# Kernel optimization log

Measured on AMD Instinct MI355X. Metric: run time of the kernel, lower is better.

## Reference

```python
import jax, jax.numpy as jnp
import numpy as np

B, S, H, E = 2, 2048, 16, 64
INV_SCALE = 8.0  # sqrt(head_dim); forward divides scores by this


def setup_inputs() -> dict:
    key = jax.random.key(0)
    ks = jax.random.split(key, 10)
    return {
        "query": jax.random.normal(ks[0], (B, S, H, E), dtype=jnp.float32),
        "key": jax.random.normal(ks[1], (B, S, H, E), dtype=jnp.float32),
        "value": jax.random.normal(ks[2], (B, S, H, E), dtype=jnp.float32),
        "attn_mask": jax.random.randint(ks[3], (B, S), 0, 2, dtype=jnp.int32),
        "Wq": jax.random.normal(ks[4], (E, E), dtype=jnp.float32) / np.sqrt(E),
        "bq": jax.random.normal(ks[5], (E,), dtype=jnp.float32) * 0.02,
        "Wk": jax.random.normal(ks[6], (E, E), dtype=jnp.float32) / np.sqrt(E),
        "bk": jax.random.normal(ks[7], (E,), dtype=jnp.float32) * 0.02,
        "Wv": jax.random.normal(ks[8], (E, E), dtype=jnp.float32) / np.sqrt(E),
        "bv": jax.random.normal(ks[9], (E,), dtype=jnp.float32) * 0.02,
    }


def reference(query, key, value, attn_mask, Wq, bq, Wk, bk, Wv, bv):
    # Linear projections over the last (embed) dim; torch Linear: x @ W.T + b
    q = jnp.einsum('bshe,fe->bhsf', query, Wq) + bq  # [B,H,S,E] (permute 0,2,1,3 fused)
    k = jnp.einsum('bshe,fe->bhsf', key, Wk) + bk
    v = jnp.einsum('bshe,fe->bhsf', value, Wv) + bv
    scores = jnp.einsum('bhqe,bhke->bhqk', q, k) / INV_SCALE  # [B,H,S,S]
    # mask: positions where attn_mask == 0 get -inf, broadcast over (1,1,k_len)
    masked = attn_mask[:, None, None, :] == 0  # [B,1,1,S]
    scores = jnp.where(masked, -jnp.inf, scores)
    attn = jax.nn.softmax(scores, axis=-1)
    out = jnp.einsum('bhqk,bhke->bqhe', attn, v)  # permute back to [B,S,H,E]
    return out
```

## Files before the change

kernel.cpp:

```cpp
#include <hip/hip_runtime.h>


#define BATCH 2
#define SEQ   2048
#define NH    16
#define DE    64
#define LDP   72
#define LDOF  68
#define NKT   (SEQ / 64)
#define QT    256
#define LOG2E 1.44269504088896340736f

using bf16x8   = __attribute__((ext_vector_type(8))) __bf16;
using bf16x4   = __attribute__((ext_vector_type(4))) __bf16;
using floatx4  = __attribute__((ext_vector_type(4))) float;
using floatx16 = __attribute__((ext_vector_type(16))) float;
using ushortx4 = __attribute__((ext_vector_type(4))) unsigned short;
using ushortx8 = __attribute__((ext_vector_type(8))) unsigned short;

__device__ __forceinline__ ushortx4 cvt4(floatx4 f) {
    bf16x4 h = __builtin_convertvector(f, bf16x4);
    return __builtin_bit_cast(ushortx4, h);
}

__device__ __forceinline__ void glds16(const unsigned short* g, unsigned short* l) {
    __builtin_amdgcn_global_load_lds(
        (const __attribute__((address_space(1))) unsigned int*)g,
        (__attribute__((address_space(3))) unsigned int*)l, 16, 0, 0);
}

__global__ __launch_bounds__(256) void proj_kernel(
    const float* __restrict__ xq, const float* __restrict__ xk, const float* __restrict__ xv,
    const float* __restrict__ Wq, const float* __restrict__ bq,
    const float* __restrict__ Wk, const float* __restrict__ bk,
    const float* __restrict__ Wv, const float* __restrict__ bv,
    unsigned short* __restrict__ qb, unsigned short* __restrict__ kb,
    unsigned short* __restrict__ vtb)
{
    __shared__ __align__(16) unsigned short Xb[64 * LDP];
    __shared__ __align__(16) unsigned short Wb[64 * LDP];
    __shared__ __align__(16) unsigned short Ob[64 * LDP];
    __shared__ float blds[64];

    const int t  = threadIdx.x;
    const int p  = blockIdx.x >> 10;
    const int bh = (blockIdx.x >> 5) & 31;
    const int st = blockIdx.x & 31;
    const int s0 = st * 64;
    const int b  = bh >> 4, h = bh & 15;
    const int lane = t & 63, w = t >> 6, quad = lane >> 4, l16 = lane & 15;

    const float* x    = (p == 0) ? xq : (p == 1) ? xk : xv;
    const float* W    = (p == 0) ? Wq : (p == 1) ? Wk : Wv;
    const float* bias = (p == 0) ? bq : (p == 1) ? bk : bv;

    #pragma unroll
    for (int i = 0; i < 4; ++i) {
        int idx = i * 1024 + t * 4;
        int row = idx >> 6, col = idx & 63;
        floatx4 xv4 = *(const floatx4*)(x + (((size_t)(b * SEQ + s0 + row) * NH + h) * DE + col));
        *(ushortx4*)&Xb[row * LDP + col] = cvt4(xv4);
        floatx4 wv4 = *(const floatx4*)(W + row * 64 + col);
        *(ushortx4*)&Wb[row * LDP + col] = cvt4(wv4);
    }
    if (t < 64) blds[t] = bias[t];
    __syncthreads();

    if (p < 2) {
        bf16x8 a0 = *(const bf16x8*)&Wb[(w * 16 + l16) * LDP + quad * 8];
        bf16x8 a1 = *(const bf16x8*)&Wb[(w * 16 + l16) * LDP + 32 + quad * 8];
        floatx4 bf4 = *(const floatx4*)&blds[w * 16 + quad * 4];
        const float scale = (p == 0) ? 0.125f * LOG2E : 1.0f;
        #pragma unroll
        for (int nb = 0; nb < 4; ++nb) {
            bf16x8 b0 = *(const bf16x8*)&Xb[(nb * 16 + l16) * LDP + quad * 8];
            bf16x8 b1 = *(const bf16x8*)&Xb[(nb * 16 + l16) * LDP + 32 + quad * 8];
            floatx4 c = {0.f, 0.f, 0.f, 0.f};
            c = __builtin_amdgcn_mfma_f32_16x16x32_bf16(a0, b0, c, 0, 0, 0);
            c = __builtin_amdgcn_mfma_f32_16x16x32_bf16(a1, b1, c, 0, 0, 0);
            floatx4 v;
            v[0] = (c[0] + bf4[0]) * scale; v[1] = (c[1] + bf4[1]) * scale;
            v[2] = (c[2] + bf4[2]) * scale; v[3] = (c[3] + bf4[3]) * scale;
            *(ushortx4*)&Ob[(nb * 16 + l16) * LDP + w * 16 + quad * 4] = cvt4(v);
        }
    } else {
        bf16x8 a0 = *(const bf16x8*)&Xb[(w * 16 + l16) * LDP + quad * 8];
        bf16x8 a1 = *(const bf16x8*)&Xb[(w * 16 + l16) * LDP + 32 + quad * 8];
        #pragma unroll
        for (int nb = 0; nb < 4; ++nb) {
            bf16x8 b0 = *(const bf16x8*)&Wb[(nb * 16 + l16) * LDP + quad * 8];
            bf16x8 b1 = *(const bf16x8*)&Wb[(nb * 16 + l16) * LDP + 32 + quad * 8];
            floatx4 c = {0.f, 0.f, 0.f, 0.f};
            c = __builtin_amdgcn_mfma_f32_16x16x32_bf16(a0, b0, c, 0, 0, 0);
            c = __builtin_amdgcn_mfma_f32_16x16x32_bf16(a1, b1, c, 0, 0, 0);
            float bw = blds[nb * 16 + l16];
            floatx4 v;
            v[0] = c[0] + bw; v[1] = c[1] + bw; v[2] = c[2] + bw; v[3] = c[3] + bw;
            *(ushortx4*)&Ob[(nb * 16 + l16) * LDP + w * 16 + quad * 4] = cvt4(v);
        }
    }
    __syncthreads();

    #pragma unroll
    for (int j = 0; j < 2; ++j) {
        int idx = j * 256 + t;
        int row = idx >> 3, c = idx & 7;
        int cp  = (c ^ (row & 7)) * 8;
        ushortx8 v = *(const ushortx8*)&Ob[row * LDP + c * 8];
        if (p < 2) {
            unsigned short* dst = (p == 0) ? qb : kb;
            *(ushortx8*)(dst + ((size_t)bh * SEQ + s0 + row) * DE + cp) = v;
        } else {
            *(ushortx8*)(vtb + ((size_t)bh * DE + row) * SEQ + s0 + cp) = v;
        }
    }
}

__global__ __launch_bounds__(512) void attn_kernel(
    const unsigned short* __restrict__ qb, const unsigned short* __restrict__ kb,
    const unsigned short* __restrict__ vtb, const int* __restrict__ mask,
    float* __restrict__ out)
{
    __shared__ __align__(16) char smem[16384 + 16384 + 36864 + 512];
    unsigned short* Kl = (unsigned short*)smem;
    unsigned short* Vl = (unsigned short*)(smem + 16384);
    unsigned short* Pq = (unsigned short*)(smem + 32768);
    float*          Ml = (float*)(smem + 32768 + 36864);
    float*          Ol = (float*)smem;

    const int t  = threadIdx.x;
    const int qt = blockIdx.x, bh = blockIdx.y;
    const int b  = bh >> 4, h = bh & 15;
    const int q0 = qt * QT;
    const int lane = t & 63, w = t >> 6;
    const int l31 = lane & 31, hl = lane >> 5;
    const int sw  = l31 & 7;
    const int qrow = w * 32 + l31;

    const unsigned short* kbase = kb + (size_t)bh * SEQ * DE;
    const unsigned short* vbase = vtb + (size_t)bh * DE * SEQ;
    const unsigned short* qsrc  = qb + ((size_t)bh * SEQ + q0) * DE;
    const int* mrow = mask + b * SEQ;

    #pragma unroll
    for (int u = 0; u < 4; ++u)
        glds16(qsrc + (u * 8 + w) * 512 + lane * 8, Pq + (u * 8 + w) * 512);
    glds16(kbase + (size_t)(w * 8 + (lane >> 3)) * DE + (lane & 7) * 8,  Kl + w * 512);
    glds16(vbase + (size_t)(w * 8 + (lane >> 3)) * SEQ + (lane & 7) * 8, Vl + w * 512);
    if (t < 64) Ml[t] = mrow[t] ? -16.0f : -1e30f;
    int mreg = (t < 64) ? mrow[64 + t] : 0;
    __syncthreads();

    bf16x8 qf[4];
    #pragma unroll
    for (int estep = 0; estep < 4; ++estep)
        qf[estep] = *(const bf16x8*)&Pq[qrow * 64 + (((2 * estep + hl) ^ sw) * 8)];

    float l_i = 0.f;
    floatx16 oacc[2];
    #pragma unroll
    for (int eh = 0; eh < 2; ++eh)
        #pragma unroll
        for (int r = 0; r < 16; ++r) oacc[eh][r] = 0.f;
    __syncthreads();

    for (int kt = 0; kt < NKT; ++kt) {
        const int cur = kt & 1, nxt = cur ^ 1;
        const unsigned short* Kc = Kl + cur * 4096;
        const unsigned short* Vc = Vl + cur * 4096;
        const float*          Mc = Ml + cur * 64;

        if (kt + 1 < NKT) {
            const int k1 = (kt + 1) * 64;
            glds16(kbase + (size_t)(k1 + w * 8 + (lane >> 3)) * DE + (lane & 7) * 8,
                   Kl + nxt * 4096 + w * 512);
            glds16(vbase + (size_t)(w * 8 + (lane >> 3)) * SEQ + k1 + (lane & 7) * 8,
                   Vl + nxt * 4096 + w * 512);
            if (t < 64) Ml[nxt * 64 + t] = mreg ? -16.0f : -1e30f;
            mreg = (t < 64 && kt + 2 < NKT) ? mrow[(kt + 2) * 64 + t] : 0;
        }

        float sum = 0.f;
        #pragma unroll
        for (int kh = 0; kh < 2; ++kh) {
            floatx16 c;
            #pragma unroll
            for (int g = 0; g < 4; ++g) {
                floatx4 mg = *(const floatx4*)&Mc[kh * 32 + g * 8 + hl * 4];
                c[g * 4 + 0] = mg[0]; c[g * 4 + 1] = mg[1];
                c[g * 4 + 2] = mg[2]; c[g * 4 + 3] = mg[3];
            }
            #pragma unroll
            for (int estep = 0; estep < 4; ++estep) {
                bf16x8 kf = *(const bf16x8*)&Kc[(kh * 32 + l31) * 64 + (((2 * estep + hl) ^ sw) * 8)];
                c = __builtin_amdgcn_mfma_f32_32x32x16_bf16(kf, qf[estep], c, 0, 0, 0);
            }
            #pragma unroll
            for (int r = 0; r < 16; ++r) {
                c[r] = __builtin_amdgcn_exp2f(c[r]);
                sum += c[r];
            }
            #pragma unroll
            for (int m = 0; m < 4; ++m) {
                floatx4 g4 = {c[4 * m + 0], c[4 * m + 1], c[4 * m + 2], c[4 * m + 3]};
                *(ushortx4*)&Pq[qrow * LDP + (4 * kh + m) * 8 + hl * 4] = cvt4(g4);
            }
        }
        sum += __shfl_xor(sum, 32);
        l_i += sum;
        __asm__ volatile("s_waitcnt lgkmcnt(0)" ::: "memory");

        bf16x8 pf[4];
        #pragma unroll
        for (int kstep = 0; kstep < 4; ++kstep)
            pf[kstep] = *(const bf16x8*)&Pq[qrow * LDP + (2 * kstep + hl) * 8];

        #pragma unroll
        for (int eh = 0; eh < 2; ++eh)
            #pragma unroll
            for (int kstep = 0; kstep < 4; ++kstep) {
                bf16x8 vf = *(const bf16x8*)&Vc[(eh * 32 + l31) * 64 + (((2 * kstep + hl) ^ sw) * 8)];
                oacc[eh] = __builtin_amdgcn_mfma_f32_32x32x16_bf16(vf, pf[kstep], oacc[eh], 0, 0, 0);
            }

        __syncthreads();
    }

    float invl = __builtin_amdgcn_rcpf(l_i);
    #pragma unroll
    for (int eh = 0; eh < 2; ++eh)
        #pragma unroll
        for (int m = 0; m < 4; ++m) {
            floatx4 ov;
            ov[0] = oacc[eh][4 * m + 0] * invl; ov[1] = oacc[eh][4 * m + 1] * invl;
            ov[2] = oacc[eh][4 * m + 2] * invl; ov[3] = oacc[eh][4 * m + 3] * invl;
            *(floatx4*)&Ol[qrow * LDOF + eh * 32 + m * 8 + hl * 4] = ov;
        }
    __syncthreads();
    #pragma unroll
    for (int pass = 0; pass < 8; ++pass) {
        int idx = pass * 512 + t;
        int rl  = idx >> 4;
        int col = (idx & 15) * 4;
        floatx4 tv = *(const floatx4*)&Ol[rl * LDOF + col];
        *(floatx4*)(out + (((size_t)b * SEQ + q0 + rl) * NH + h) * DE + col) = tv;
    }
}

extern "C" void kernel_launch(void* const* d_in, const int* in_sizes, int n_in,
                              void* d_out, int out_size, void* d_ws, size_t ws_size,
                              hipStream_t stream) {
    const float* query = (const float*)d_in[0];
    const float* key   = (const float*)d_in[1];
    const float* value = (const float*)d_in[2];
    const int*   mask  = (const int*)d_in[3];
    const float* Wq = (const float*)d_in[4];
    const float* bq = (const float*)d_in[5];
    const float* Wk = (const float*)d_in[6];
    const float* bk = (const float*)d_in[7];
    const float* Wv = (const float*)d_in[8];
    const float* bv = (const float*)d_in[9];

    const size_t tensor_elems = (size_t)BATCH * NH * SEQ * DE;
    unsigned short* qb  = (unsigned short*)d_ws;
    unsigned short* kb  = qb + tensor_elems;
    unsigned short* vtb = kb + tensor_elems;

    proj_kernel<<<dim3(3 * BATCH * NH * (SEQ / 64)), 256, 0, stream>>>(
        query, key, value, Wq, bq, Wk, bk, Wv, bv, qb, kb, vtb);
    attn_kernel<<<dim3(SEQ / QT, BATCH * NH), 512, 0, stream>>>(
        qb, kb, vtb, mask, (float*)d_out);
}
```

Baseline: 156.8 us.

## Preload full mask bias, hoist K/V fragment loads, unroll double-buffered loop

The whole mask row is converted to additive bias in shared memory once at kernel start, which removes the per-tile mask loads and stores from the loop. All K and V fragments for a tile are now read from LDS into registers before the next tile's async global-to-LDS loads are issued. The key loop is unrolled by two with separate named buffers, so buffer addresses are compile-time constants. The epilogue reuses the P/Q buffer to stage output in two halves. The main cost is higher register pressure from holding 16 bf16x8 fragments at the same time.

```diff
diff --git a/kernel.cpp b/kernel.cpp
--- a/kernel.cpp
+++ b/kernel.cpp
@@ -15,6 +15,7 @@
 using bf16x4   = __attribute__((ext_vector_type(4))) __bf16;
 using floatx4  = __attribute__((ext_vector_type(4))) float;
 using floatx16 = __attribute__((ext_vector_type(16))) float;
+using intx4    = __attribute__((ext_vector_type(4))) int;
 using ushortx4 = __attribute__((ext_vector_type(4))) unsigned short;
 using ushortx8 = __attribute__((ext_vector_type(8))) unsigned short;
 
@@ -121,12 +122,10 @@
     const unsigned short* __restrict__ vtb, const int* __restrict__ mask,
     float* __restrict__ out)
 {
-    __shared__ __align__(16) char smem[16384 + 16384 + 36864 + 512];
-    unsigned short* Kl = (unsigned short*)smem;
-    unsigned short* Vl = (unsigned short*)(smem + 16384);
-    unsigned short* Pq = (unsigned short*)(smem + 32768);
-    float*          Ml = (float*)(smem + 32768 + 36864);
-    float*          Ol = (float*)smem;
+    __shared__ __align__(64) unsigned short K0[64 * 64], K1[64 * 64];
+    __shared__ __align__(64) unsigned short V0[64 * 64], V1[64 * 64];
+    __shared__ __align__(64) unsigned short Pq[QT * LDP];
+    __shared__ __align__(64) float Mall[SEQ];
 
     const int t  = threadIdx.x;
     const int qt = blockIdx.x, bh = blockIdx.y;
@@ -145,16 +144,22 @@
     #pragma unroll
     for (int u = 0; u < 4; ++u)
         glds16(qsrc + (u * 8 + w) * 512 + lane * 8, Pq + (u * 8 + w) * 512);
-    glds16(kbase + (size_t)(w * 8 + (lane >> 3)) * DE + (lane & 7) * 8,  Kl + w * 512);
-    glds16(vbase + (size_t)(w * 8 + (lane >> 3)) * SEQ + (lane & 7) * 8, Vl + w * 512);
-    if (t < 64) Ml[t] = mrow[t] ? -16.0f : -1e30f;
-    int mreg = (t < 64) ? mrow[64 + t] : 0;
+    glds16(kbase + (size_t)(w * 8 + (lane >> 3)) * DE + (lane & 7) * 8,  K0 + w * 512);
+    glds16(vbase + (size_t)(w * 8 + (lane >> 3)) * SEQ + (lane & 7) * 8, V0 + w * 512);
+    {
+        intx4 mv = *(const intx4*)(mrow + t * 4);
+        floatx4 bias;
+        bias[0] = mv[0] ? -16.0f : -1e30f; bias[1] = mv[1] ? -16.0f : -1e30f;
+        bias[2] = mv[2] ? -16.0f : -1e30f; bias[3] = mv[3] ? -16.0f : -1e30f;
+        *(floatx4*)&Mall[t * 4] = bias;
+    }
     __syncthreads();
 
     bf16x8 qf[4];
     #pragma unroll
     for (int estep = 0; estep < 4; ++estep)
         qf[estep] = *(const bf16x8*)&Pq[qrow * 64 + (((2 * estep + hl) ^ sw) * 8)];
+    __syncthreads();
 
     float l_i = 0.f;
     floatx16 oacc[2];
@@ -162,24 +167,32 @@
     for (int eh = 0; eh < 2; ++eh)
         #pragma unroll
         for (int r = 0; r < 16; ++r) oacc[eh][r] = 0.f;
-    __syncthreads();
-
-    for (int kt = 0; kt < NKT; ++kt) {
-        const int cur = kt & 1, nxt = cur ^ 1;
-        const unsigned short* Kc = Kl + cur * 4096;
-        const unsigned short* Vc = Vl + cur * 4096;
-        const float*          Mc = Ml + cur * 64;
+
+    auto body = [&](int kt, const unsigned short* Kc, const unsigned short* Vc,
+                    unsigned short* Kn, unsigned short* Vn) {
+        bf16x8 kf[8], vf[8];
+        #pragma unroll
+        for (int kh = 0; kh < 2; ++kh)
+            #pragma unroll
+            for (int estep = 0; estep < 4; ++estep)
+                kf[kh * 4 + estep] =
+                    *(const bf16x8*)&Kc[(kh * 32 + l31) * 64 + (((2 * estep + hl) ^ sw) * 8)];
+        #pragma unroll
+        for (int eh = 0; eh < 2; ++eh)
+            #pragma unroll
+            for (int kstep = 0; kstep < 4; ++kstep)
+                vf[eh * 4 + kstep] =
+                    *(const bf16x8*)&Vc[(eh * 32 + l31) * 64 + (((2 * kstep + hl) ^ sw) * 8)];
 
         if (kt + 1 < NKT) {
             const int k1 = (kt + 1) * 64;
             glds16(kbase + (size_t)(k1 + w * 8 + (lane >> 3)) * DE + (lane & 7) * 8,
-                   Kl + nxt * 4096 + w * 512);
+                   Kn + w * 512);
             glds16(vbase + (size_t)(w * 8 + (lane >> 3)) * SEQ + k1 + (lane & 7) * 8,
-                   Vl + nxt * 4096 + w * 512);
-            if (t < 64) Ml[nxt * 64 + t] = mreg ? -16.0f : -1e30f;
-            mreg = (t < 64 && kt + 2 < NKT) ? mrow[(kt + 2) * 64 + t] : 0;
-        }
-
+                   Vn + w * 512);
+        }
+
+        const float* Mc = &Mall[kt * 64];
         float sum = 0.f;
         #pragma unroll
         for (int kh = 0; kh < 2; ++kh) {
@@ -191,10 +204,8 @@
                 c[g * 4 + 2] = mg[2]; c[g * 4 + 3] = mg[3];
             }
             #pragma unroll
-            for (int estep = 0; estep < 4; ++estep) {
-                bf16x8 kf = *(const bf16x8*)&Kc[(kh * 32 + l31) * 64 + (((2 * estep + hl) ^ sw) * 8)];
-                c = __builtin_amdgcn_mfma_f32_32x32x16_bf16(kf, qf[estep], c, 0, 0, 0);
-            }
+            for (int estep = 0; estep < 4; ++estep)
+                c = __builtin_amdgcn_mfma_f32_32x32x16_bf16(kf[kh * 4 + estep], qf[estep], c, 0, 0, 0);
             #pragma unroll
             for (int r = 0; r < 16; ++r) {
                 c[r] = __builtin_amdgcn_exp2f(c[r]);
@@ -214,36 +225,47 @@
         #pragma unroll
         for (int kstep = 0; kstep < 4; ++kstep)
             pf[kstep] = *(const bf16x8*)&Pq[qrow * LDP + (2 * kstep + hl) * 8];
-
         #pragma unroll
         for (int eh = 0; eh < 2; ++eh)
             #pragma unroll
-            for (int kstep = 0; kstep < 4; ++kstep) {
-                bf16x8 vf = *(const bf16x8*)&Vc[(eh * 32 + l31) * 64 + (((2 * kstep + hl) ^ sw) * 8)];
-                oacc[eh] = __builtin_amdgcn_mfma_f32_32x32x16_bf16(vf, pf[kstep], oacc[eh], 0, 0, 0);
-            }
+            for (int kstep = 0; kstep < 4; ++kstep)
+                oacc[eh] = __builtin_amdgcn_mfma_f32_32x32x16_bf16(vf[eh * 4 + kstep], pf[kstep],
+                                                                   oacc[eh], 0, 0, 0);
 
         __syncthreads();
+    };
+
+    for (int kt = 0; kt < NKT; kt += 2) {
+        body(kt,     K0, V0, K1, V1);
+        body(kt + 1, K1, V1, K0, V0);
     }
 
     float invl = __builtin_amdgcn_rcpf(l_i);
-    #pragma unroll
-    for (int eh = 0; eh < 2; ++eh)
-        #pragma unroll
-        for (int m = 0; m < 4; ++m) {
-            floatx4 ov;
-            ov[0] = oacc[eh][4 * m + 0] * invl; ov[1] = oacc[eh][4 * m + 1] * invl;
-            ov[2] = oacc[eh][4 * m + 2] * invl; ov[3] = oacc[eh][4 * m + 3] * invl;
-            *(floatx4*)&Ol[qrow * LDOF + eh * 32 + m * 8 + hl * 4] = ov;
-        }
-    __syncthreads();
-    #pragma unroll
-    for (int pass = 0; pass < 8; ++pass) {
-        int idx = pass * 512 + t;
-        int rl  = idx >> 4;
-        int col = (idx & 15) * 4;
-        floatx4 tv = *(const floatx4*)&Ol[rl * LDOF + col];
-        *(floatx4*)(out + (((size_t)b * SEQ + q0 + rl) * NH + h) * DE + col) = tv;
+    float* Ol = (float*)Pq;
+    #pragma unroll
+    for (int half = 0; half < 2; ++half) {
+        __syncthreads();
+        if ((w >> 2) == half) {
+            int qr = qrow - half * 128;
+            #pragma unroll
+            for (int eh = 0; eh < 2; ++eh)
+                #pragma unroll
+                for (int m = 0; m < 4; ++m) {
+                    floatx4 ov;
+                    ov[0] = oacc[eh][4 * m + 0] * invl; ov[1] = oacc[eh][4 * m + 1] * invl;
+                    ov[2] = oacc[eh][4 * m + 2] * invl; ov[3] = oacc[eh][4 * m + 3] * invl;
+                    *(floatx4*)&Ol[qr * LDOF + eh * 32 + m * 8 + hl * 4] = ov;
+                }
+        }
+        __syncthreads();
+        #pragma unroll
+        for (int pass = 0; pass < 4; ++pass) {
+            int idx = pass * 512 + t;
+            int rl  = idx >> 4;
+            int col = (idx & 15) * 4;
+            floatx4 tv = *(const floatx4*)&Ol[rl * LDOF + col];
+            *(floatx4*)(out + (((size_t)b * SEQ + q0 + half * 128 + rl) * NH + h) * DE + col) = tv;
+        }
     }
 }
 
```

After: 158.1 us. No clear change (+0.8%).
